# Performance work log

Hardware: AMD Instinct MI355X
Metric: run time of the kernel (lower is better)

The kernel has to match this reference:

```python
import jax, jax.numpy as jnp
import numpy as np

R_SELF = 0.1  # config.r_self from the 'GENERAL' preset


def setup_inputs() -> dict:
    key = jax.random.key(0)
    k1, k2 = jax.random.split(key)
    N, M, D = 16384, 8192, 128
    x = jax.random.uniform(k1, (N, D), dtype=jnp.float32)
    self_samples = jax.random.uniform(k2, (M, D), dtype=jnp.float32)
    return {"x": x, "self_samples": self_samples}


def _cdist(a, b):
    # Euclidean pairwise distances, same math as torch.cdist(p=2).
    a2 = jnp.sum(a * a, axis=1, keepdims=True)          # [N,1]
    b2 = jnp.sum(b * b, axis=1)[None, :]                # [1,M]
    d2 = a2 + b2 - 2.0 * (a @ b.T)                      # [N,M]
    return jnp.sqrt(jnp.maximum(d2, 0.0))


def reference(x, self_samples):
    # get_anomaly_score: min over self set, shifted by r_self, clamped at 0.
    min_dist_to_self = jnp.min(_cdist(x, self_samples), axis=1)  # [N]
    score = jnp.maximum(min_dist_to_self - R_SELF, 0.0)
    return score
```

## Files before the change

kernel.cpp:

```cpp
#include <hip/hip_runtime.h>


using half_t = _Float16;
typedef _Float16 half8 __attribute__((ext_vector_type(8)));
typedef _Float16 half2v __attribute__((ext_vector_type(2)));
typedef float floatx16 __attribute__((ext_vector_type(16)));

#define TILE_ELEMS (128 * 128)

__device__ __forceinline__ void async_load16(const void* g, void* l) {
    __builtin_amdgcn_global_load_lds(
        (const __attribute__((address_space(1))) void*)g,
        (__attribute__((address_space(3))) void*)l, 16, 0, 0);
}

__device__ __forceinline__ void stage_tile(const half_t* __restrict__ Bt,
                                           half_t* __restrict__ dst, int tid) {
    #pragma unroll
    for (int j = 0; j < 4; ++j) {
        int chunk = j * 512 + tid;
        async_load16(Bt + (size_t)chunk * 8, dst + (size_t)chunk * 8);
    }
}

__device__ __forceinline__ half2v h2min(half2v a, half2v b) {
    return __builtin_elementwise_min(a, b);
}

__device__ __forceinline__ half2v pkrtz(float lo, float hi) {
    auto t = __builtin_amdgcn_cvt_pkrtz(lo, hi);
    return __builtin_bit_cast(half2v, t);
}

__global__ __launch_bounds__(256) void prep_kernel(
    const float* __restrict__ x, const float* __restrict__ self,
    half_t* __restrict__ Aws, half_t* __restrict__ Bws,
    float* __restrict__ b2h, float* __restrict__ a2, int Atiles)
{
    __shared__ float part[256];
    int tile = blockIdx.x;
    int tid  = threadIdx.x;
    bool isB = tile >= Atiles;
    int bt   = tile - Atiles;
    const float* src = isB ? (self + (size_t)bt * TILE_ELEMS)
                           : (x    + (size_t)tile * TILE_ELEMS);
    half_t* dst = isB ? (Bws + (size_t)bt * TILE_ELEMS)
                      : (Aws + (size_t)tile * TILE_ELEMS);
    float sgn = isB ? 1.f : -1.f;

    int rowt = tid & 127;
    int k8b  = tid >> 7;
    float ss = 0.f;
    #pragma unroll
    for (int i = 0; i < 8; ++i) {
        int k8 = i * 2 + k8b;
        const float4* p = (const float4*)(src + rowt * 128 + k8 * 8);
        float4 f0 = p[0];
        float4 f1 = p[1];
        half8 h;
        h[0] = (half_t)(sgn * f0.x); h[1] = (half_t)(sgn * f0.y);
        h[2] = (half_t)(sgn * f0.z); h[3] = (half_t)(sgn * f0.w);
        h[4] = (half_t)(sgn * f1.x); h[5] = (half_t)(sgn * f1.y);
        h[6] = (half_t)(sgn * f1.z); h[7] = (half_t)(sgn * f1.w);
        *(half8*)(dst + (size_t)(i * 256 + tid) * 8) = h;
        ss += f0.x*f0.x + f0.y*f0.y + f0.z*f0.z + f0.w*f0.w;
        ss += f1.x*f1.x + f1.y*f1.y + f1.z*f1.z + f1.w*f1.w;
    }
    part[tid] = ss;
    __syncthreads();
    if (tid < 128) {
        float tot = part[tid] + part[tid + 128];
        if (isB) b2h[bt * 128 + tid] = 0.5f * tot;
        else     a2[tile * 128 + tid] = tot;
    }
}

template<int VN>
__device__ __forceinline__ void gemm_iter(
    int t, int iters, int tid, int wc, int ln31, int lh,
    const half_t* __restrict__ Bbase, half_t (*ring)[TILE_ELEMS],
    const float* __restrict__ b2sh,
    const half8 (&areg)[4][8], half2v (&minacc)[4][8])
{
    __builtin_amdgcn_sched_barrier(0);
    if constexpr (VN == 4) asm volatile("s_waitcnt vmcnt(4)" ::: "memory");
    else                   asm volatile("s_waitcnt vmcnt(0)" ::: "memory");
    asm volatile("s_waitcnt lgkmcnt(0)" ::: "memory");
    __builtin_amdgcn_s_barrier();
    __builtin_amdgcn_sched_barrier(0);

    if (t + 2 < iters)
        stage_tile(Bbase + (size_t)(t + 2) * TILE_ELEMS, &ring[(t + 2) % 3][0], tid);

    const half_t* Bs = &ring[t % 3][0];
    float b2v = b2sh[t * 128 + wc * 32 + ln31];

    half8 bf[8];
    #pragma unroll
    for (int ki = 0; ki < 8; ++ki)
        bf[ki] = *(const half8*)(Bs + (size_t)((ki * 2 + lh) * 128 + wc * 32 + ln31) * 8);

    floatx16 c0;
    #pragma unroll
    for (int r = 0; r < 16; ++r) c0[r] = b2v;

    #pragma unroll
    for (int rp = 0; rp < 2; ++rp) {
        floatx16 a0 = __builtin_amdgcn_mfma_f32_32x32x16_f16(areg[rp * 2][0],     bf[0], c0, 0, 0, 0);
        floatx16 a1 = __builtin_amdgcn_mfma_f32_32x32x16_f16(areg[rp * 2 + 1][0], bf[0], c0, 0, 0, 0);
        #pragma unroll
        for (int ki = 1; ki < 8; ++ki) {
            a0 = __builtin_amdgcn_mfma_f32_32x32x16_f16(areg[rp * 2][ki],     bf[ki], a0, 0, 0, 0);
            a1 = __builtin_amdgcn_mfma_f32_32x32x16_f16(areg[rp * 2 + 1][ki], bf[ki], a1, 0, 0, 0);
        }
        #pragma unroll
        for (int i = 0; i < 8; ++i) {
            minacc[rp * 2][i]     = h2min(minacc[rp * 2][i],     pkrtz(a0[2 * i], a0[2 * i + 1]));
            minacc[rp * 2 + 1][i] = h2min(minacc[rp * 2 + 1][i], pkrtz(a1[2 * i], a1[2 * i + 1]));
        }
    }
}

__global__ __launch_bounds__(512, 2) void min_gemm_kernel(
    const half_t* __restrict__ Aws, const half_t* __restrict__ Bws,
    const float* __restrict__ b2h, float* __restrict__ Pmin, int Mslice)
{
    __shared__ half_t ring[3][TILE_ELEMS];
    __shared__ float  b2sh[2048];

    int tid  = threadIdx.x;
    int lane = tid & 63;
    int wid  = tid >> 6;
    int wr   = wid >> 2;
    int wc   = wid & 3;
    int ln31 = lane & 31, lh = lane >> 5;

    const half_t* Atile = Aws + (size_t)(blockIdx.x * 2 + wr) * TILE_ELEMS;
    half8 areg[4][8];
    #pragma unroll
    for (int rt = 0; rt < 4; ++rt)
        #pragma unroll
        for (int ki = 0; ki < 8; ++ki)
            areg[rt][ki] = *(const half8*)(
                Atile + (size_t)((ki * 2 + lh) * 128 + rt * 32 + ln31) * 8);

    int s = blockIdx.y;
    for (int j = tid; j < Mslice; j += 512)
        b2sh[j] = b2h[s * Mslice + j];

    half2v minacc[4][8];
    const half_t HMAX = (half_t)65504.f;
    #pragma unroll
    for (int rt = 0; rt < 4; ++rt)
        #pragma unroll
        for (int i = 0; i < 8; ++i) { minacc[rt][i][0] = HMAX; minacc[rt][i][1] = HMAX; }

    int iters = Mslice >> 7;
    const half_t* Bbase = Bws + (size_t)s * iters * TILE_ELEMS;

    __syncthreads();

    stage_tile(Bbase,              &ring[0][0], tid);
    stage_tile(Bbase + TILE_ELEMS, &ring[1][0], tid);

    for (int t = 0; t < iters - 1; ++t)
        gemm_iter<4>(t, iters, tid, wc, ln31, lh, Bbase, ring, b2sh, areg, minacc);
    gemm_iter<0>(iters - 1, iters, tid, wc, ln31, lh, Bbase, ring, b2sh, areg, minacc);

    #pragma unroll
    for (int rt = 0; rt < 4; ++rt)
        #pragma unroll
        for (int i = 0; i < 8; ++i) {
            int m = __builtin_bit_cast(int, minacc[rt][i]);
            #pragma unroll
            for (int x = 1; x < 32; x <<= 1) {
                int o = __shfl_xor(m, x, 64);
                m = __builtin_bit_cast(int,
                        h2min(__builtin_bit_cast(half2v, m),
                              __builtin_bit_cast(half2v, o)));
            }
            if (ln31 == 0) {
                half2v mv = __builtin_bit_cast(half2v, m);
                int r0 = 2 * i, r1 = 2 * i + 1;
                int rowb = blockIdx.x * 256 + wr * 128 + rt * 32 + 4 * lh;
                int row0 = rowb + (r0 & 3) + 8 * (r0 >> 2);
                int row1 = rowb + (r1 & 3) + 8 * (r1 >> 2);
                Pmin[(size_t)row0 * 16 + s * 4 + wc] = (float)mv[0];
                Pmin[(size_t)row1 * 16 + s * 4 + wc] = (float)mv[1];
            }
        }
}

__global__ __launch_bounds__(256) void final_kernel(
    const float* __restrict__ a2, const float* __restrict__ Pmin,
    float* __restrict__ out)
{
    int row = blockIdx.x * 256 + threadIdx.x;
    const float4* pp = (const float4*)(Pmin + (size_t)row * 16);
    float4 p0 = pp[0];
    float4 p1 = pp[1];
    float4 p2 = pp[2];
    float4 p3 = pp[3];
    float q0 = fminf(fminf(p0.x, p0.y), fminf(p0.z, p0.w));
    float q1 = fminf(fminf(p1.x, p1.y), fminf(p1.z, p1.w));
    float q2 = fminf(fminf(p2.x, p2.y), fminf(p2.z, p2.w));
    float q3 = fminf(fminf(p3.x, p3.y), fminf(p3.z, p3.w));
    float p  = fminf(fminf(q0, q1), fminf(q2, q3));
    float d2 = a2[row] + 2.f * p;
    float d  = sqrtf(fmaxf(d2, 0.f));
    out[row] = fmaxf(d - 0.1f, 0.f);
}

extern "C" void kernel_launch(void* const* d_in, const int* in_sizes, int n_in,
                              void* d_out, int out_size, void* d_ws, size_t ws_size,
                              hipStream_t stream)
{
    const float* x    = (const float*)d_in[0];
    const float* self = (const float*)d_in[1];
    float* out        = (float*)d_out;

    int N = in_sizes[0] / 128;
    int M = in_sizes[1] / 128;
    int Atiles = N / 128;
    int Btiles = M / 128;

    char* w      = (char*)d_ws;
    half_t* Aws  = (half_t*)w;
    half_t* Bws  = Aws + (size_t)N * 128;
    float*  b2h  = (float*)(w + (size_t)(N + M) * 128 * 2);
    float*  Pmin = b2h + M;
    float*  a2   = Pmin + (size_t)N * 16;

    prep_kernel<<<Atiles + Btiles, 256, 0, stream>>>(x, self, Aws, Bws, b2h, a2, Atiles);

    int Mslice = M / 4;
    dim3 grid(N / 256, 4);
    min_gemm_kernel<<<grid, 512, 0, stream>>>(Aws, Bws, b2h, Pmin, Mslice);

    final_kernel<<<N / 256, 256, 0, stream>>>(a2, Pmin, out);
}
```

Before: 103.0 us.

## Give each wave a private double-buffered B slice to drop block barriers

```diff
diff --git a/kernel.cpp b/kernel.cpp
--- a/kernel.cpp
+++ b/kernel.cpp
@@ -14,12 +14,14 @@
         (__attribute__((address_space(3))) void*)l, 16, 0, 0);
 }
 
-__device__ __forceinline__ void stage_tile(const half_t* __restrict__ Bt,
-                                           half_t* __restrict__ dst, int tid) {
-    #pragma unroll
-    for (int j = 0; j < 4; ++j) {
-        int chunk = j * 512 + tid;
-        async_load16(Bt + (size_t)chunk * 8, dst + (size_t)chunk * 8);
+__device__ __forceinline__ void stage_slice(const half_t* __restrict__ Bt,
+                                            half_t* __restrict__ dst,
+                                            int wc, int lane) {
+    int l5 = lane >> 5, l31 = lane & 31;
+    #pragma unroll
+    for (int c = 0; c < 8; ++c) {
+        const half_t* src = Bt + (size_t)((c * 2 + l5) * 128 + wc * 32 + l31) * 8;
+        async_load16(src, dst + (size_t)c * 512);
     }
 }
 
@@ -77,33 +79,29 @@
 
 template<int VN>
 __device__ __forceinline__ void gemm_iter(
-    int t, int iters, int tid, int wc, int ln31, int lh,
-    const half_t* __restrict__ Bbase, half_t (*ring)[TILE_ELEMS],
+    int t, int iters, int wc, int lane, int ln31, int lh,
+    const half_t* __restrict__ Bbase,
+    half_t* __restrict__ buf0, half_t* __restrict__ buf1,
     const float* __restrict__ b2sh,
     const half8 (&areg)[4][8], half2v (&minacc)[4][8])
 {
+    if constexpr (VN == 8) asm volatile("s_waitcnt vmcnt(8)" ::: "memory");
+    else                   asm volatile("s_waitcnt vmcnt(0)" ::: "memory");
     __builtin_amdgcn_sched_barrier(0);
-    if constexpr (VN == 4) asm volatile("s_waitcnt vmcnt(4)" ::: "memory");
-    else                   asm volatile("s_waitcnt vmcnt(0)" ::: "memory");
-    asm volatile("s_waitcnt lgkmcnt(0)" ::: "memory");
-    __builtin_amdgcn_s_barrier();
-    __builtin_amdgcn_sched_barrier(0);
-
-    if (t + 2 < iters)
-        stage_tile(Bbase + (size_t)(t + 2) * TILE_ELEMS, &ring[(t + 2) % 3][0], tid);
-
-    const half_t* Bs = &ring[t % 3][0];
+
+    const half_t* Bs = (t & 1) ? buf1 : buf0;
     float b2v = b2sh[t * 128 + wc * 32 + ln31];
 
     half8 bf[8];
     #pragma unroll
     for (int ki = 0; ki < 8; ++ki)
-        bf[ki] = *(const half8*)(Bs + (size_t)((ki * 2 + lh) * 128 + wc * 32 + ln31) * 8);
+        bf[ki] = *(const half8*)(Bs + (size_t)((ki * 2 + lh) * 32 + ln31) * 8);
 
     floatx16 c0;
     #pragma unroll
     for (int r = 0; r < 16; ++r) c0[r] = b2v;
 
+    __builtin_amdgcn_s_setprio(1);
     #pragma unroll
     for (int rp = 0; rp < 2; ++rp) {
         floatx16 a0 = __builtin_amdgcn_mfma_f32_32x32x16_f16(areg[rp * 2][0],     bf[0], c0, 0, 0, 0);
@@ -119,23 +117,27 @@
             minacc[rp * 2 + 1][i] = h2min(minacc[rp * 2 + 1][i], pkrtz(a1[2 * i], a1[2 * i + 1]));
         }
     }
-}
-
-__global__ __launch_bounds__(512, 2) void min_gemm_kernel(
+    __builtin_amdgcn_s_setprio(0);
+
+    __builtin_amdgcn_sched_barrier(0);
+    if (t + 2 < iters)
+        stage_slice(Bbase + (size_t)(t + 2) * TILE_ELEMS,
+                    (t & 1) ? buf1 : buf0, wc, lane);
+}
+
+__global__ __launch_bounds__(256, 2) void min_gemm_kernel(
     const half_t* __restrict__ Aws, const half_t* __restrict__ Bws,
     const float* __restrict__ b2h, float* __restrict__ Pmin, int Mslice)
 {
-    __shared__ half_t ring[3][TILE_ELEMS];
+    __shared__ half_t slices[4][2][4096];
     __shared__ float  b2sh[2048];
 
     int tid  = threadIdx.x;
     int lane = tid & 63;
-    int wid  = tid >> 6;
-    int wr   = wid >> 2;
-    int wc   = wid & 3;
+    int wc   = tid >> 6;
     int ln31 = lane & 31, lh = lane >> 5;
 
-    const half_t* Atile = Aws + (size_t)(blockIdx.x * 2 + wr) * TILE_ELEMS;
+    const half_t* Atile = Aws + (size_t)blockIdx.x * TILE_ELEMS;
     half8 areg[4][8];
     #pragma unroll
     for (int rt = 0; rt < 4; ++rt)
@@ -145,7 +147,7 @@
                 Atile + (size_t)((ki * 2 + lh) * 128 + rt * 32 + ln31) * 8);
 
     int s = blockIdx.y;
-    for (int j = tid; j < Mslice; j += 512)
+    for (int j = tid; j < Mslice; j += 256)
         b2sh[j] = b2h[s * Mslice + j];
 
     half2v minacc[4][8];
@@ -160,12 +162,15 @@
 
     __syncthreads();
 
-    stage_tile(Bbase,              &ring[0][0], tid);
-    stage_tile(Bbase + TILE_ELEMS, &ring[1][0], tid);
+    half_t* buf0 = &slices[wc][0][0];
+    half_t* buf1 = &slices[wc][1][0];
+
+    stage_slice(Bbase,              buf0, wc, lane);
+    stage_slice(Bbase + TILE_ELEMS, buf1, wc, lane);
 
     for (int t = 0; t < iters - 1; ++t)
-        gemm_iter<4>(t, iters, tid, wc, ln31, lh, Bbase, ring, b2sh, areg, minacc);
-    gemm_iter<0>(iters - 1, iters, tid, wc, ln31, lh, Bbase, ring, b2sh, areg, minacc);
+        gemm_iter<8>(t, iters, wc, lane, ln31, lh, Bbase, buf0, buf1, b2sh, areg, minacc);
+    gemm_iter<0>(iters - 1, iters, wc, lane, ln31, lh, Bbase, buf0, buf1, b2sh, areg, minacc);
 
     #pragma unroll
     for (int rt = 0; rt < 4; ++rt)
@@ -182,7 +187,7 @@
             if (ln31 == 0) {
                 half2v mv = __builtin_bit_cast(half2v, m);
                 int r0 = 2 * i, r1 = 2 * i + 1;
-                int rowb = blockIdx.x * 256 + wr * 128 + rt * 32 + 4 * lh;
+                int rowb = blockIdx.x * 128 + rt * 32 + 4 * lh;
                 int row0 = rowb + (r0 & 3) + 8 * (r0 >> 2);
                 int row1 = rowb + (r1 & 3) + 8 * (r1 >> 2);
                 Pmin[(size_t)row0 * 16 + s * 4 + wc] = (float)mv[0];
@@ -234,8 +239,8 @@
     prep_kernel<<<Atiles + Btiles, 256, 0, stream>>>(x, self, Aws, Bws, b2h, a2, Atiles);
 
     int Mslice = M / 4;
-    dim3 grid(N / 256, 4);
-    min_gemm_kernel<<<grid, 512, 0, stream>>>(Aws, Bws, b2h, Pmin, Mslice);
+    dim3 grid(N / 128, 4);
+    min_gemm_kernel<<<grid, 256, 0, stream>>>(Aws, Bws, b2h, Pmin, Mslice);
 
     final_kernel<<<N / 256, 256, 0, stream>>>(a2, Pmin, out);
 }
```

Measured after the change: 110.4 us. 7.2% more time.

## Shrink GEMM blocks to 128 rows with 64-column B tiles and double buffering

Applied to the files above, without the earlier changes.

```diff
diff --git a/kernel.cpp b/kernel.cpp
--- a/kernel.cpp
+++ b/kernel.cpp
@@ -14,12 +14,13 @@
         (__attribute__((address_space(3))) void*)l, 16, 0, 0);
 }
 
-__device__ __forceinline__ void stage_tile(const half_t* __restrict__ Bt,
-                                           half_t* __restrict__ dst, int tid) {
+__device__ __forceinline__ void stage_tile64(const half_t* __restrict__ base,
+                                             half_t* __restrict__ dst, int tid) {
     #pragma unroll
     for (int j = 0; j < 4; ++j) {
-        int chunk = j * 512 + tid;
-        async_load16(Bt + (size_t)chunk * 8, dst + (size_t)chunk * 8);
+        int c = j * 256 + tid;
+        const half_t* src = base + (size_t)(c + (c >> 6) * 64) * 8;
+        async_load16(src, dst + (size_t)c * 8);
     }
 }
 
@@ -75,100 +76,79 @@
     }
 }
 
-template<int VN>
-__device__ __forceinline__ void gemm_iter(
-    int t, int iters, int tid, int wc, int ln31, int lh,
-    const half_t* __restrict__ Bbase, half_t (*ring)[TILE_ELEMS],
-    const float* __restrict__ b2sh,
-    const half8 (&areg)[4][8], half2v (&minacc)[4][8])
-{
-    __builtin_amdgcn_sched_barrier(0);
-    if constexpr (VN == 4) asm volatile("s_waitcnt vmcnt(4)" ::: "memory");
-    else                   asm volatile("s_waitcnt vmcnt(0)" ::: "memory");
-    asm volatile("s_waitcnt lgkmcnt(0)" ::: "memory");
-    __builtin_amdgcn_s_barrier();
-    __builtin_amdgcn_sched_barrier(0);
-
-    if (t + 2 < iters)
-        stage_tile(Bbase + (size_t)(t + 2) * TILE_ELEMS, &ring[(t + 2) % 3][0], tid);
-
-    const half_t* Bs = &ring[t % 3][0];
-    float b2v = b2sh[t * 128 + wc * 32 + ln31];
-
-    half8 bf[8];
-    #pragma unroll
-    for (int ki = 0; ki < 8; ++ki)
-        bf[ki] = *(const half8*)(Bs + (size_t)((ki * 2 + lh) * 128 + wc * 32 + ln31) * 8);
-
-    floatx16 c0;
-    #pragma unroll
-    for (int r = 0; r < 16; ++r) c0[r] = b2v;
-
-    #pragma unroll
-    for (int rp = 0; rp < 2; ++rp) {
-        floatx16 a0 = __builtin_amdgcn_mfma_f32_32x32x16_f16(areg[rp * 2][0],     bf[0], c0, 0, 0, 0);
-        floatx16 a1 = __builtin_amdgcn_mfma_f32_32x32x16_f16(areg[rp * 2 + 1][0], bf[0], c0, 0, 0, 0);
-        #pragma unroll
-        for (int ki = 1; ki < 8; ++ki) {
-            a0 = __builtin_amdgcn_mfma_f32_32x32x16_f16(areg[rp * 2][ki],     bf[ki], a0, 0, 0, 0);
-            a1 = __builtin_amdgcn_mfma_f32_32x32x16_f16(areg[rp * 2 + 1][ki], bf[ki], a1, 0, 0, 0);
-        }
-        #pragma unroll
-        for (int i = 0; i < 8; ++i) {
-            minacc[rp * 2][i]     = h2min(minacc[rp * 2][i],     pkrtz(a0[2 * i], a0[2 * i + 1]));
-            minacc[rp * 2 + 1][i] = h2min(minacc[rp * 2 + 1][i], pkrtz(a1[2 * i], a1[2 * i + 1]));
-        }
-    }
-}
-
-__global__ __launch_bounds__(512, 2) void min_gemm_kernel(
+__global__ __launch_bounds__(256, 4) void min_gemm_kernel(
     const half_t* __restrict__ Aws, const half_t* __restrict__ Bws,
     const float* __restrict__ b2h, float* __restrict__ Pmin, int Mslice)
 {
-    __shared__ half_t ring[3][TILE_ELEMS];
-    __shared__ float  b2sh[2048];
+    __shared__ half_t bufs[2][16 * 64 * 8];
+    __shared__ float  b2sh[1024];
 
     int tid  = threadIdx.x;
     int lane = tid & 63;
     int wid  = tid >> 6;
-    int wr   = wid >> 2;
-    int wc   = wid & 3;
+    int wr   = wid >> 1;
+    int wc   = wid & 1;
     int ln31 = lane & 31, lh = lane >> 5;
 
-    const half_t* Atile = Aws + (size_t)(blockIdx.x * 2 + wr) * TILE_ELEMS;
-    half8 areg[4][8];
-    #pragma unroll
-    for (int rt = 0; rt < 4; ++rt)
+    const half_t* Atile = Aws + (size_t)blockIdx.x * TILE_ELEMS;
+    half8 areg[2][8];
+    #pragma unroll
+    for (int rt = 0; rt < 2; ++rt)
         #pragma unroll
         for (int ki = 0; ki < 8; ++ki)
             areg[rt][ki] = *(const half8*)(
-                Atile + (size_t)((ki * 2 + lh) * 128 + rt * 32 + ln31) * 8);
+                Atile + (size_t)((ki * 2 + lh) * 128 + wr * 64 + rt * 32 + ln31) * 8);
 
     int s = blockIdx.y;
-    for (int j = tid; j < Mslice; j += 512)
-        b2sh[j] = b2h[s * Mslice + j];
-
-    half2v minacc[4][8];
+    for (int j = tid; j < 1024; j += 256)
+        b2sh[j] = b2h[s * 1024 + j];
+
+    half2v minacc[2][8];
     const half_t HMAX = (half_t)65504.f;
     #pragma unroll
-    for (int rt = 0; rt < 4; ++rt)
+    for (int rt = 0; rt < 2; ++rt)
         #pragma unroll
         for (int i = 0; i < 8; ++i) { minacc[rt][i][0] = HMAX; minacc[rt][i][1] = HMAX; }
 
-    int iters = Mslice >> 7;
-    const half_t* Bbase = Bws + (size_t)s * iters * TILE_ELEMS;
-
-    __syncthreads();
-
-    stage_tile(Bbase,              &ring[0][0], tid);
-    stage_tile(Bbase + TILE_ELEMS, &ring[1][0], tid);
-
-    for (int t = 0; t < iters - 1; ++t)
-        gemm_iter<4>(t, iters, tid, wc, ln31, lh, Bbase, ring, b2sh, areg, minacc);
-    gemm_iter<0>(iters - 1, iters, tid, wc, ln31, lh, Bbase, ring, b2sh, areg, minacc);
-
-    #pragma unroll
-    for (int rt = 0; rt < 4; ++rt)
+    int iters = Mslice >> 6;
+    const half_t* Bslice = Bws + (size_t)s * 8 * TILE_ELEMS;
+
+    stage_tile64(Bslice, &bufs[0][0], tid);
+
+    for (int t = 0; t < iters; ++t) {
+        asm volatile("s_waitcnt vmcnt(0)" ::: "memory");
+        __builtin_amdgcn_s_barrier();
+        __builtin_amdgcn_sched_barrier(0);
+
+        if (t + 1 < iters) {
+            const half_t* nb = Bslice + (size_t)((t + 1) >> 1) * TILE_ELEMS
+                             + (size_t)(((t + 1) & 1) * 64) * 8;
+            stage_tile64(nb, &bufs[(t + 1) & 1][0], tid);
+        }
+
+        const half_t* Bs = &bufs[t & 1][0];
+        float b2v = b2sh[t * 64 + wc * 32 + ln31];
+
+        floatx16 acc0, acc1;
+        #pragma unroll
+        for (int r = 0; r < 16; ++r) { acc0[r] = b2v; acc1[r] = b2v; }
+
+        #pragma unroll
+        for (int ki = 0; ki < 8; ++ki) {
+            half8 bf = *(const half8*)(Bs + (size_t)((ki * 2 + lh) * 64 + wc * 32 + ln31) * 8);
+            acc0 = __builtin_amdgcn_mfma_f32_32x32x16_f16(areg[0][ki], bf, acc0, 0, 0, 0);
+            acc1 = __builtin_amdgcn_mfma_f32_32x32x16_f16(areg[1][ki], bf, acc1, 0, 0, 0);
+        }
+
+        #pragma unroll
+        for (int i = 0; i < 8; ++i) {
+            minacc[0][i] = h2min(minacc[0][i], pkrtz(acc0[2 * i], acc0[2 * i + 1]));
+            minacc[1][i] = h2min(minacc[1][i], pkrtz(acc1[2 * i], acc1[2 * i + 1]));
+        }
+    }
+
+    #pragma unroll
+    for (int rt = 0; rt < 2; ++rt)
         #pragma unroll
         for (int i = 0; i < 8; ++i) {
             int m = __builtin_bit_cast(int, minacc[rt][i]);
@@ -182,11 +162,11 @@
             if (ln31 == 0) {
                 half2v mv = __builtin_bit_cast(half2v, m);
                 int r0 = 2 * i, r1 = 2 * i + 1;
-                int rowb = blockIdx.x * 256 + wr * 128 + rt * 32 + 4 * lh;
+                int rowb = blockIdx.x * 128 + wr * 64 + rt * 32 + 4 * lh;
                 int row0 = rowb + (r0 & 3) + 8 * (r0 >> 2);
                 int row1 = rowb + (r1 & 3) + 8 * (r1 >> 2);
-                Pmin[(size_t)row0 * 16 + s * 4 + wc] = (float)mv[0];
-                Pmin[(size_t)row1 * 16 + s * 4 + wc] = (float)mv[1];
+                Pmin[(size_t)row0 * 16 + s * 2 + wc] = (float)mv[0];
+                Pmin[(size_t)row1 * 16 + s * 2 + wc] = (float)mv[1];
             }
         }
 }
@@ -233,9 +213,9 @@
 
     prep_kernel<<<Atiles + Btiles, 256, 0, stream>>>(x, self, Aws, Bws, b2h, a2, Atiles);
 
-    int Mslice = M / 4;
-    dim3 grid(N / 256, 4);
-    min_gemm_kernel<<<grid, 512, 0, stream>>>(Aws, Bws, b2h, Pmin, Mslice);
+    int Mslice = M / 8;
+    dim3 grid(N / 128, 8);
+    min_gemm_kernel<<<grid, 256, 0, stream>>>(Aws, Bws, b2h, Pmin, Mslice);
 
     final_kernel<<<N / 256, 256, 0, stream>>>(a2, Pmin, out);
 }
```

Result: no change. 102.3 us (-0.8%).

## Interleave B-tile staging with MFMA phases, add setprio and block swizzle

Applied to the files above, without the earlier changes.

```diff
diff --git a/kernel.cpp b/kernel.cpp
--- a/kernel.cpp
+++ b/kernel.cpp
@@ -7,6 +7,7 @@
 typedef float floatx16 __attribute__((ext_vector_type(16)));
 
 #define TILE_ELEMS (128 * 128)
+#define MFMA16 __builtin_amdgcn_mfma_f32_32x32x16_f16
 
 __device__ __forceinline__ void async_load16(const void* g, void* l) {
     __builtin_amdgcn_global_load_lds(
@@ -14,13 +15,11 @@
         (__attribute__((address_space(3))) void*)l, 16, 0, 0);
 }
 
-__device__ __forceinline__ void stage_tile(const half_t* __restrict__ Bt,
-                                           half_t* __restrict__ dst, int tid) {
-    #pragma unroll
-    for (int j = 0; j < 4; ++j) {
-        int chunk = j * 512 + tid;
-        async_load16(Bt + (size_t)chunk * 8, dst + (size_t)chunk * 8);
-    }
+__device__ __forceinline__ void stage_chunk(const half_t* __restrict__ Bt,
+                                            half_t* __restrict__ dst,
+                                            int p, int tid) {
+    int c = p * 512 + tid;
+    async_load16(Bt + (size_t)c * 8, dst + (size_t)c * 8);
 }
 
 __device__ __forceinline__ half2v h2min(half2v a, half2v b) {
@@ -76,7 +75,7 @@
 }
 
 template<int VN>
-__device__ __forceinline__ void gemm_iter(
+__device__ __forceinline__ void tile_iter(
     int t, int iters, int tid, int wc, int ln31, int lh,
     const half_t* __restrict__ Bbase, half_t (*ring)[TILE_ELEMS],
     const float* __restrict__ b2sh,
@@ -85,39 +84,57 @@
     __builtin_amdgcn_sched_barrier(0);
     if constexpr (VN == 4) asm volatile("s_waitcnt vmcnt(4)" ::: "memory");
     else                   asm volatile("s_waitcnt vmcnt(0)" ::: "memory");
-    asm volatile("s_waitcnt lgkmcnt(0)" ::: "memory");
-    __builtin_amdgcn_s_barrier();
     __builtin_amdgcn_sched_barrier(0);
 
-    if (t + 2 < iters)
-        stage_tile(Bbase + (size_t)(t + 2) * TILE_ELEMS, &ring[(t + 2) % 3][0], tid);
-
-    const half_t* Bs = &ring[t % 3][0];
+    const half_t* Bs  = &ring[t % 3][0];
+    half_t*       stq = &ring[(t + 2) % 3][0];
+    const half_t* Bn  = Bbase + (size_t)(t + 2) * TILE_ELEMS;
+    bool dost = (t + 2 < iters);
+
     float b2v = b2sh[t * 128 + wc * 32 + ln31];
-
-    half8 bf[8];
-    #pragma unroll
-    for (int ki = 0; ki < 8; ++ki)
-        bf[ki] = *(const half8*)(Bs + (size_t)((ki * 2 + lh) * 128 + wc * 32 + ln31) * 8);
-
     floatx16 c0;
     #pragma unroll
     for (int r = 0; r < 16; ++r) c0[r] = b2v;
 
-    #pragma unroll
-    for (int rp = 0; rp < 2; ++rp) {
-        floatx16 a0 = __builtin_amdgcn_mfma_f32_32x32x16_f16(areg[rp * 2][0],     bf[0], c0, 0, 0, 0);
-        floatx16 a1 = __builtin_amdgcn_mfma_f32_32x32x16_f16(areg[rp * 2 + 1][0], bf[0], c0, 0, 0, 0);
-        #pragma unroll
-        for (int ki = 1; ki < 8; ++ki) {
-            a0 = __builtin_amdgcn_mfma_f32_32x32x16_f16(areg[rp * 2][ki],     bf[ki], a0, 0, 0, 0);
-            a1 = __builtin_amdgcn_mfma_f32_32x32x16_f16(areg[rp * 2 + 1][ki], bf[ki], a1, 0, 0, 0);
+    floatx16 acc0, acc1, acc2, acc3;
+
+    #pragma unroll
+    for (int p = 0; p < 4; ++p) {
+        half8 bfa = *(const half8*)(Bs + (size_t)(((2*p)   * 2 + lh) * 128 + wc * 32 + ln31) * 8);
+        half8 bfb = *(const half8*)(Bs + (size_t)(((2*p+1) * 2 + lh) * 128 + wc * 32 + ln31) * 8);
+        if (dost) stage_chunk(Bn, stq, p, tid);
+
+        __builtin_amdgcn_s_barrier();
+        asm volatile("s_waitcnt lgkmcnt(0)" ::: "memory");
+        __builtin_amdgcn_sched_barrier(0);
+
+        __builtin_amdgcn_s_setprio(1);
+        if (p == 0) {
+            acc0 = MFMA16(areg[0][0], bfa, c0, 0, 0, 0);
+            acc1 = MFMA16(areg[1][0], bfa, c0, 0, 0, 0);
+            acc2 = MFMA16(areg[2][0], bfa, c0, 0, 0, 0);
+            acc3 = MFMA16(areg[3][0], bfa, c0, 0, 0, 0);
+        } else {
+            acc0 = MFMA16(areg[0][2*p], bfa, acc0, 0, 0, 0);
+            acc1 = MFMA16(areg[1][2*p], bfa, acc1, 0, 0, 0);
+            acc2 = MFMA16(areg[2][2*p], bfa, acc2, 0, 0, 0);
+            acc3 = MFMA16(areg[3][2*p], bfa, acc3, 0, 0, 0);
         }
-        #pragma unroll
-        for (int i = 0; i < 8; ++i) {
-            minacc[rp * 2][i]     = h2min(minacc[rp * 2][i],     pkrtz(a0[2 * i], a0[2 * i + 1]));
-            minacc[rp * 2 + 1][i] = h2min(minacc[rp * 2 + 1][i], pkrtz(a1[2 * i], a1[2 * i + 1]));
-        }
+        acc0 = MFMA16(areg[0][2*p+1], bfb, acc0, 0, 0, 0);
+        acc1 = MFMA16(areg[1][2*p+1], bfb, acc1, 0, 0, 0);
+        acc2 = MFMA16(areg[2][2*p+1], bfb, acc2, 0, 0, 0);
+        acc3 = MFMA16(areg[3][2*p+1], bfb, acc3, 0, 0, 0);
+        __builtin_amdgcn_s_setprio(0);
+        __builtin_amdgcn_sched_barrier(0);
+        __builtin_amdgcn_s_barrier();
+    }
+
+    #pragma unroll
+    for (int i = 0; i < 8; ++i) {
+        minacc[0][i] = h2min(minacc[0][i], pkrtz(acc0[2*i], acc0[2*i+1]));
+        minacc[1][i] = h2min(minacc[1][i], pkrtz(acc1[2*i], acc1[2*i+1]));
+        minacc[2][i] = h2min(minacc[2][i], pkrtz(acc2[2*i], acc2[2*i+1]));
+        minacc[3][i] = h2min(minacc[3][i], pkrtz(acc3[2*i], acc3[2*i+1]));
     }
 }
 
@@ -135,7 +152,12 @@
     int wc   = wid & 3;
     int ln31 = lane & 31, lh = lane >> 5;
 
-    const half_t* Atile = Aws + (size_t)(blockIdx.x * 2 + wr) * TILE_ELEMS;
+    int id  = blockIdx.x + gridDim.x * blockIdx.y;
+    int swz = (id & 7) * 32 + (id >> 3);
+    int bx  = swz & 63;
+    int s   = swz >> 6;
+
+    const half_t* Atile = Aws + (size_t)(bx * 2 + wr) * TILE_ELEMS;
     half8 areg[4][8];
     #pragma unroll
     for (int rt = 0; rt < 4; ++rt)
@@ -144,8 +166,7 @@
             areg[rt][ki] = *(const half8*)(
                 Atile + (size_t)((ki * 2 + lh) * 128 + rt * 32 + ln31) * 8);
 
-    int s = blockIdx.y;
-    for (int j = tid; j < Mslice; j += 512)
+    for (int j = tid; j < 2048; j += 512)
         b2sh[j] = b2h[s * Mslice + j];
 
     half2v minacc[4][8];
@@ -160,12 +181,14 @@
 
     __syncthreads();
 
-    stage_tile(Bbase,              &ring[0][0], tid);
-    stage_tile(Bbase + TILE_ELEMS, &ring[1][0], tid);
+    #pragma unroll
+    for (int p = 0; p < 4; ++p) stage_chunk(Bbase,              &ring[0][0], p, tid);
+    #pragma unroll
+    for (int p = 0; p < 4; ++p) stage_chunk(Bbase + TILE_ELEMS, &ring[1][0], p, tid);
 
     for (int t = 0; t < iters - 1; ++t)
-        gemm_iter<4>(t, iters, tid, wc, ln31, lh, Bbase, ring, b2sh, areg, minacc);
-    gemm_iter<0>(iters - 1, iters, tid, wc, ln31, lh, Bbase, ring, b2sh, areg, minacc);
+        tile_iter<4>(t, iters, tid, wc, ln31, lh, Bbase, ring, b2sh, areg, minacc);
+    tile_iter<0>(iters - 1, iters, tid, wc, ln31, lh, Bbase, ring, b2sh, areg, minacc);
 
     #pragma unroll
     for (int rt = 0; rt < 4; ++rt)
@@ -182,7 +205,7 @@
             if (ln31 == 0) {
                 half2v mv = __builtin_bit_cast(half2v, m);
                 int r0 = 2 * i, r1 = 2 * i + 1;
-                int rowb = blockIdx.x * 256 + wr * 128 + rt * 32 + 4 * lh;
+                int rowb = bx * 256 + wr * 128 + rt * 32 + 4 * lh;
                 int row0 = rowb + (r0 & 3) + 8 * (r0 >> 2);
                 int row1 = rowb + (r1 & 3) + 8 * (r1 >> 2);
                 Pmin[(size_t)row0 * 16 + s * 4 + wc] = (float)mv[0];
```

After: 107.1 us. 3.9% more time.
